# Kernel tuning notes

Hardware: AMD Instinct MI355X
Metric: run time of the kernel (lower is better)

Reference implementation:

```python
import jax, jax.numpy as jnp
import numpy as np

GAMMA = 0.99
BETA = 0.01
B, T, A = 65536, 128, 8


def setup_inputs() -> dict:
    key = jax.random.key(0)
    ks = jax.random.split(key, 6)
    return {
        "values": jax.random.normal(ks[0], (B, T), jnp.float32),
        "last_value": jax.random.normal(ks[1], (B,), jnp.float32),
        "rewards": jax.random.normal(ks[2], (B, T), jnp.float32),
        "log_probs": -jax.nn.softplus(jax.random.normal(ks[3], (B, T, A), jnp.float32)),
        "entropies": jax.random.uniform(ks[4], (B, T, A), jnp.float32),
        "terminal_mask": jax.random.randint(ks[5], (B,), 0, 2) > 0,
    }


def _a3c_loss(values, last_value, rewards, log_probs, entropies, terminal_mask):
    # Bootstrap value R: zero if terminal, else detached last-state value
    R0 = jnp.where(terminal_mask, 0.0, jax.lax.stop_gradient(last_value))  # [B]
    values_next = jnp.concatenate([values[:, 1:], R0[:, None]], axis=1)    # [B,T] = values[i+1]
    lp = log_probs.sum(-1)    # [B,T], log_probs[i].sum()
    ent = entropies.sum(-1)   # [B,T], entropies[i].sum()

    # scan over time (reverse), xs laid out time-major: [T, B]
    xs = (rewards.T, values.T, values_next.T, lp.T, ent.T)
    z = jnp.zeros((values.shape[0],), values.dtype)

    def step(carry, x):
        R, gae, actor, critic = carry
        r, v, v_next, l, e = x
        R = GAMMA * R + r
        adv = R - v
        critic = critic + 0.5 * adv * adv
        delta = r + GAMMA * v_next - v
        gae = gae * GAMMA + delta
        actor = actor - l * jax.lax.stop_gradient(gae) - BETA * e
        return (R, gae, actor, critic), None

    (R, gae, actor, critic), _ = jax.lax.scan(step, (R0, z, z, z), xs, reverse=True)
    return jnp.stack([actor, critic], axis=-1)  # [B, 2]: (actor_loss, critic_loss)


def reference(values, last_value, rewards, log_probs, entropies, terminal_mask):
    return _a3c_loss(values, last_value, rewards, log_probs, entropies, terminal_mask)
```

## Files before the change

kernel.cpp:

```cpp
#include <hip/hip_runtime.h>

#define GAMMA 0.99f
#define BETA  0.01f

typedef const __attribute__((address_space(1))) void GVoid;
typedef __attribute__((address_space(3))) void LVoid;

__global__ __launch_bounds__(256, 4) void a3c_loss_kernel(
    const float* __restrict__ values,
    const float* __restrict__ last_value,
    const float* __restrict__ rewards,
    const float* __restrict__ log_probs,
    const float* __restrict__ entropies,
    const int*   __restrict__ terminal_mask,
    float* __restrict__ out,
    int B)
{
    __shared__ float lds_stage[4][2048];

    const int wave = threadIdx.x >> 6;
    const int lane = threadIdx.x & 63;
    const int b = blockIdx.x * 4 + wave;
    if (b >= B) return;

    const float2 v2 = reinterpret_cast<const float2*>(values  + (size_t)b * 128)[lane];
    const float2 r2 = reinterpret_cast<const float2*>(rewards + (size_t)b * 128)[lane];
    const float lv  = last_value[b];
    const int   tm  = terminal_mask[b];

    const float4* lp4 = reinterpret_cast<const float4*>(log_probs + (size_t)b * 1024);
    const float4* en4 = reinterpret_cast<const float4*>(entropies + (size_t)b * 1024);
    float* wbase = &lds_stage[wave][0];
    #pragma unroll
    for (int k = 0; k < 4; ++k) {
        __builtin_amdgcn_global_load_lds((GVoid*)(lp4 + lane + 64 * k),
                                         (LVoid*)(wbase + 256 * k + lane * 4),
                                         16, 0, 0);
    }
    #pragma unroll
    for (int k = 0; k < 4; ++k) {
        __builtin_amdgcn_global_load_lds((GVoid*)(en4 + lane + 64 * k),
                                         (LVoid*)(wbase + 1024 + 256 * k + lane * 4),
                                         16, 0, 0);
    }
    __builtin_amdgcn_sched_barrier(0);

    const float v0 = v2.x, v1 = v2.y;
    const float r0 = r2.x, r1 = r2.y;

    const float R0 = (tm != 0) ? 0.0f : lv;

    float vnext1 = __shfl_down(v0, 1, 64);
    if (lane == 63) vnext1 = R0;
    const float delta1 = r1 + GAMMA * vnext1 - v1;
    const float delta0 = r0 + GAMMA * v1    - v0;

    float m  = GAMMA * GAMMA;
    float cR = fmaf(GAMMA, r1, r0);
    float cG = fmaf(GAMMA, delta1, delta0);

    #pragma unroll
    for (int d = 1; d < 64; d <<= 1) {
        const float om  = __shfl_down(m,  d, 64);
        const float ocR = __shfl_down(cR, d, 64);
        const float ocG = __shfl_down(cG, d, 64);
        if (lane + d < 64) {
            cR = fmaf(m, ocR, cR);
            cG = fmaf(m, ocG, cG);
            m  = m * om;
        }
    }
    float pm  = __shfl_down(m,  1, 64);
    float pcR = __shfl_down(cR, 1, 64);
    float pcG = __shfl_down(cG, 1, 64);
    if (lane == 63) { pm = 1.0f; pcR = 0.0f; pcG = 0.0f; }

    const float Rin = fmaf(pm, R0, pcR);
    const float gin = pcG;

    const float R1   = fmaf(GAMMA, Rin, r1);
    const float Rt0  = fmaf(GAMMA, R1,  r0);
    const float adv1 = R1  - v1;
    const float adv0 = Rt0 - v0;
    float critic = 0.5f * (adv1 * adv1 + adv0 * adv0);

    const float g1 = fmaf(GAMMA, gin, delta1);
    const float g0 = fmaf(GAMMA, g1,  delta0);

    const int par = (lane >> 1) & 1;
    const int hb  = lane >> 2;
    const int h1 = hb + 16;
    const int h2 = hb + 32;
    const int h3 = hb + 48;
    const float gA0 = __shfl(g0, hb, 64), gB0 = __shfl(g1, hb, 64);
    const float gA1 = __shfl(g0, h1, 64), gB1 = __shfl(g1, h1, 64);
    const float gA2 = __shfl(g0, h2, 64), gB2 = __shfl(g1, h2, 64);
    const float gA3 = __shfl(g0, h3, 64), gB3 = __shfl(g1, h3, 64);
    const float gk0 = par ? gB0 : gA0;
    const float gk1 = par ? gB1 : gA1;
    const float gk2 = par ? gB2 : gA2;
    const float gk3 = par ? gB3 : gA3;

    asm volatile("s_waitcnt vmcnt(0)" ::: "memory");
    __builtin_amdgcn_sched_barrier(0);

    const float4* lpL = reinterpret_cast<const float4*>(wbase);
    const float4* enL = reinterpret_cast<const float4*>(wbase + 1024);
    const float4 L0 = lpL[lane      ];
    const float4 L1 = lpL[lane +  64];
    const float4 L2 = lpL[lane + 128];
    const float4 L3 = lpL[lane + 192];
    const float4 E0 = enL[lane      ];
    const float4 E1 = enL[lane +  64];
    const float4 E2 = enL[lane + 128];
    const float4 E3 = enL[lane + 192];

    const float sL0 = (L0.x + L0.y) + (L0.z + L0.w);
    const float sL1 = (L1.x + L1.y) + (L1.z + L1.w);
    const float sL2 = (L2.x + L2.y) + (L2.z + L2.w);
    const float sL3 = (L3.x + L3.y) + (L3.z + L3.w);
    float actor = -(sL0 * gk0 + sL1 * gk1 + sL2 * gk2 + sL3 * gk3);

    const float esum = ((E0.x + E0.y) + (E0.z + E0.w)) + ((E1.x + E1.y) + (E1.z + E1.w))
                     + ((E2.x + E2.y) + (E2.z + E2.w)) + ((E3.x + E3.y) + (E3.z + E3.w));
    actor = fmaf(-BETA, esum, actor);

    #pragma unroll
    for (int d = 32; d >= 1; d >>= 1) {
        actor  += __shfl_down(actor,  d, 64);
        critic += __shfl_down(critic, d, 64);
    }

    if (lane == 0) {
        reinterpret_cast<float2*>(out)[b] = make_float2(actor, critic);
    }
}

extern "C" void kernel_launch(void* const* d_in, const int* in_sizes, int n_in,
                              void* d_out, int out_size, void* d_ws, size_t ws_size,
                              hipStream_t stream) {
    const float* values      = (const float*)d_in[0];
    const float* last_value  = (const float*)d_in[1];
    const float* rewards     = (const float*)d_in[2];
    const float* log_probs   = (const float*)d_in[3];
    const float* entropies   = (const float*)d_in[4];
    const int*   terminal    = (const int*)d_in[5];
    float* out = (float*)d_out;

    const int B = in_sizes[1];
    const int blocks = (B + 3) / 4;

    a3c_loss_kernel<<<blocks, 256, 0, stream>>>(
        values, last_value, rewards, log_probs, entropies, terminal, out, B);
}
```

Measured before the change: 539.5 us.

## Process 32 rows per wave with double-buffered async LDS staging

Each wave now handles 32 consecutive rows instead of one. It uses two LDS buffers, so the async global-to-LDS loads for the next row (log_probs, entropies, values, rewards, last_value, mask) are in flight while the current row's scan and reduction run. The launch grid shrinks by 32x and occupancy is lowered to 2 blocks per CU to fit the doubled LDS footprint. This amortises launch and scheduling overhead and overlaps memory with compute. The cost is fewer concurrent waves, which can reduce the memory parallelism available to the hardware.

```diff
diff --git a/kernel.cpp b/kernel.cpp
--- a/kernel.cpp
+++ b/kernel.cpp
@@ -6,7 +6,15 @@
 typedef const __attribute__((address_space(1))) void GVoid;
 typedef __attribute__((address_space(3))) void LVoid;
 
-__global__ __launch_bounds__(256, 4) void a3c_loss_kernel(
+#define BUF_FLOATS 2432
+#define ROWS_PER_WAVE 32
+
+#define WAITV(N) do { \
+    asm volatile("s_waitcnt vmcnt(" #N ")" ::: "memory"); \
+    __builtin_amdgcn_sched_barrier(0); \
+} while (0)
+
+__global__ __launch_bounds__(256, 2) void a3c_loss_kernel(
     const float* __restrict__ values,
     const float* __restrict__ last_value,
     const float* __restrict__ rewards,
@@ -16,124 +24,148 @@
     float* __restrict__ out,
     int B)
 {
-    __shared__ float lds_stage[4][2048];
+    __shared__ float lds[4][2][BUF_FLOATS];
 
     const int wave = threadIdx.x >> 6;
     const int lane = threadIdx.x & 63;
-    const int b = blockIdx.x * 4 + wave;
-    if (b >= B) return;
+    const int wid  = blockIdx.x * 4 + wave;
+    const int r0   = wid * ROWS_PER_WAVE;
+    if (r0 >= B) return;
 
-    const float2 v2 = reinterpret_cast<const float2*>(values  + (size_t)b * 128)[lane];
-    const float2 r2 = reinterpret_cast<const float2*>(rewards + (size_t)b * 128)[lane];
-    const float lv  = last_value[b];
-    const int   tm  = terminal_mask[b];
+    float* const buf0 = &lds[wave][0][0];
+    float* const buf1 = &lds[wave][1][0];
 
-    const float4* lp4 = reinterpret_cast<const float4*>(log_probs + (size_t)b * 1024);
-    const float4* en4 = reinterpret_cast<const float4*>(entropies + (size_t)b * 1024);
-    float* wbase = &lds_stage[wave][0];
-    #pragma unroll
-    for (int k = 0; k < 4; ++k) {
-        __builtin_amdgcn_global_load_lds((GVoid*)(lp4 + lane + 64 * k),
-                                         (LVoid*)(wbase + 256 * k + lane * 4),
-                                         16, 0, 0);
+    auto stage = [&](float* buf, int row) {
+        row = (row < B) ? row : (B - 1);
+        const size_t rb = (size_t)row;
+        const float4* lp4 = reinterpret_cast<const float4*>(log_probs + rb * 1024) + lane;
+        const float4* en4 = reinterpret_cast<const float4*>(entropies + rb * 1024) + lane;
+        #pragma unroll
+        for (int k = 0; k < 4; ++k)
+            __builtin_amdgcn_global_load_lds((GVoid*)(lp4 + 64 * k),
+                                             (LVoid*)(buf + 256 * k), 16, 0, 0);
+        #pragma unroll
+        for (int k = 0; k < 4; ++k)
+            __builtin_amdgcn_global_load_lds((GVoid*)(en4 + 64 * k),
+                                             (LVoid*)(buf + 1024 + 256 * k), 16, 0, 0);
+        const float* vp = values  + rb * 128 + lane;
+        const float* rp = rewards + rb * 128 + lane;
+        __builtin_amdgcn_global_load_lds((GVoid*)(vp     ), (LVoid*)(buf + 2048     ), 4, 0, 0);
+        __builtin_amdgcn_global_load_lds((GVoid*)(vp + 64), (LVoid*)(buf + 2048 + 64), 4, 0, 0);
+        __builtin_amdgcn_global_load_lds((GVoid*)(rp     ), (LVoid*)(buf + 2176     ), 4, 0, 0);
+        __builtin_amdgcn_global_load_lds((GVoid*)(rp + 64), (LVoid*)(buf + 2176 + 64), 4, 0, 0);
+        __builtin_amdgcn_global_load_lds((GVoid*)(last_value    + rb), (LVoid*)(buf + 2304), 4, 0, 0);
+        __builtin_amdgcn_global_load_lds((GVoid*)(terminal_mask + rb), (LVoid*)(buf + 2368), 4, 0, 0);
+        __builtin_amdgcn_sched_barrier(0);
+    };
+
+    auto process = [&](const float* buf, int row) {
+        const float2 v2 = reinterpret_cast<const float2*>(buf + 2048)[lane];
+        const float2 r2 = reinterpret_cast<const float2*>(buf + 2176)[lane];
+        const float  lv = buf[2304 + lane];
+        const int    tm = reinterpret_cast<const int*>(buf)[2368 + lane];
+
+        const float v0 = v2.x, v1 = v2.y;
+        const float r0v = r2.x, r1v = r2.y;
+
+        const float R0 = (tm != 0) ? 0.0f : lv;
+
+        float vnext1 = __shfl_down(v0, 1, 64);
+        if (lane == 63) vnext1 = R0;
+        const float delta1 = r1v + GAMMA * vnext1 - v1;
+        const float delta0 = r0v + GAMMA * v1    - v0;
+
+        float m  = GAMMA * GAMMA;
+        float cR = fmaf(GAMMA, r1v, r0v);
+        float cG = fmaf(GAMMA, delta1, delta0);
+
+        #pragma unroll
+        for (int d = 1; d < 64; d <<= 1) {
+            const float om  = __shfl_down(m,  d, 64);
+            const float ocR = __shfl_down(cR, d, 64);
+            const float ocG = __shfl_down(cG, d, 64);
+            if (lane + d < 64) {
+                cR = fmaf(m, ocR, cR);
+                cG = fmaf(m, ocG, cG);
+                m  = m * om;
+            }
+        }
+        float pm  = __shfl_down(m,  1, 64);
+        float pcR = __shfl_down(cR, 1, 64);
+        float pcG = __shfl_down(cG, 1, 64);
+        if (lane == 63) { pm = 1.0f; pcR = 0.0f; pcG = 0.0f; }
+
+        const float Rin = fmaf(pm, R0, pcR);
+        const float gin = pcG;
+
+        const float R1   = fmaf(GAMMA, Rin, r1v);
+        const float Rt0  = fmaf(GAMMA, R1,  r0v);
+        const float adv1 = R1  - v1;
+        const float adv0 = Rt0 - v0;
+        float critic = 0.5f * (adv1 * adv1 + adv0 * adv0);
+
+        const float g1 = fmaf(GAMMA, gin, delta1);
+        const float g0 = fmaf(GAMMA, g1,  delta0);
+
+        const int par = (lane >> 1) & 1;
+        const int hb  = lane >> 2;
+        const float gA0 = __shfl(g0, hb,      64), gB0 = __shfl(g1, hb,      64);
+        const float gA1 = __shfl(g0, hb + 16, 64), gB1 = __shfl(g1, hb + 16, 64);
+        const float gA2 = __shfl(g0, hb + 32, 64), gB2 = __shfl(g1, hb + 32, 64);
+        const float gA3 = __shfl(g0, hb + 48, 64), gB3 = __shfl(g1, hb + 48, 64);
+        const float gk0 = par ? gB0 : gA0;
+        const float gk1 = par ? gB1 : gA1;
+        const float gk2 = par ? gB2 : gA2;
+        const float gk3 = par ? gB3 : gA3;
+
+        const float4* lpL = reinterpret_cast<const float4*>(buf);
+        const float4* enL = reinterpret_cast<const float4*>(buf + 1024);
+        const float4 L0 = lpL[lane      ];
+        const float4 L1 = lpL[lane +  64];
+        const float4 L2 = lpL[lane + 128];
+        const float4 L3 = lpL[lane + 192];
+        const float4 E0 = enL[lane      ];
+        const float4 E1 = enL[lane +  64];
+        const float4 E2 = enL[lane + 128];
+        const float4 E3 = enL[lane + 192];
+
+        const float sL0 = (L0.x + L0.y) + (L0.z + L0.w);
+        const float sL1 = (L1.x + L1.y) + (L1.z + L1.w);
+        const float sL2 = (L2.x + L2.y) + (L2.z + L2.w);
+        const float sL3 = (L3.x + L3.y) + (L3.z + L3.w);
+        float actor = -(sL0 * gk0 + sL1 * gk1 + sL2 * gk2 + sL3 * gk3);
+
+        const float esum = ((E0.x + E0.y) + (E0.z + E0.w)) + ((E1.x + E1.y) + (E1.z + E1.w))
+                         + ((E2.x + E2.y) + (E2.z + E2.w)) + ((E3.x + E3.y) + (E3.z + E3.w));
+        actor = fmaf(-BETA, esum, actor);
+
+        #pragma unroll
+        for (int d = 32; d >= 1; d >>= 1) {
+            actor  += __shfl_down(actor,  d, 64);
+            critic += __shfl_down(critic, d, 64);
+        }
+
+        if (lane == 0 && row < B) {
+            reinterpret_cast<float2*>(out)[row] = make_float2(actor, critic);
+        }
+        __builtin_amdgcn_sched_barrier(0);
+    };
+
+    stage(buf0, r0);
+    #pragma unroll 1
+    for (int i = 0; i < ROWS_PER_WAVE - 2; i += 2) {
+        stage(buf1, r0 + i + 1);
+        WAITV(14);
+        process(buf0, r0 + i);
+        stage(buf0, r0 + i + 2);
+        WAITV(14);
+        process(buf1, r0 + i + 1);
     }
-    #pragma unroll
-    for (int k = 0; k < 4; ++k) {
-        __builtin_amdgcn_global_load_lds((GVoid*)(en4 + lane + 64 * k),
-                                         (LVoid*)(wbase + 1024 + 256 * k + lane * 4),
-                                         16, 0, 0);
-    }
-    __builtin_amdgcn_sched_barrier(0);
-
-    const float v0 = v2.x, v1 = v2.y;
-    const float r0 = r2.x, r1 = r2.y;
-
-    const float R0 = (tm != 0) ? 0.0f : lv;
-
-    float vnext1 = __shfl_down(v0, 1, 64);
-    if (lane == 63) vnext1 = R0;
-    const float delta1 = r1 + GAMMA * vnext1 - v1;
-    const float delta0 = r0 + GAMMA * v1    - v0;
-
-    float m  = GAMMA * GAMMA;
-    float cR = fmaf(GAMMA, r1, r0);
-    float cG = fmaf(GAMMA, delta1, delta0);
-
-    #pragma unroll
-    for (int d = 1; d < 64; d <<= 1) {
-        const float om  = __shfl_down(m,  d, 64);
-        const float ocR = __shfl_down(cR, d, 64);
-        const float ocG = __shfl_down(cG, d, 64);
-        if (lane + d < 64) {
-            cR = fmaf(m, ocR, cR);
-            cG = fmaf(m, ocG, cG);
-            m  = m * om;
-        }
-    }
-    float pm  = __shfl_down(m,  1, 64);
-    float pcR = __shfl_down(cR, 1, 64);
-    float pcG = __shfl_down(cG, 1, 64);
-    if (lane == 63) { pm = 1.0f; pcR = 0.0f; pcG = 0.0f; }
-
-    const float Rin = fmaf(pm, R0, pcR);
-    const float gin = pcG;
-
-    const float R1   = fmaf(GAMMA, Rin, r1);
-    const float Rt0  = fmaf(GAMMA, R1,  r0);
-    const float adv1 = R1  - v1;
-    const float adv0 = Rt0 - v0;
-    float critic = 0.5f * (adv1 * adv1 + adv0 * adv0);
-
-    const float g1 = fmaf(GAMMA, gin, delta1);
-    const float g0 = fmaf(GAMMA, g1,  delta0);
-
-    const int par = (lane >> 1) & 1;
-    const int hb  = lane >> 2;
-    const int h1 = hb + 16;
-    const int h2 = hb + 32;
-    const int h3 = hb + 48;
-    const float gA0 = __shfl(g0, hb, 64), gB0 = __shfl(g1, hb, 64);
-    const float gA1 = __shfl(g0, h1, 64), gB1 = __shfl(g1, h1, 64);
-    const float gA2 = __shfl(g0, h2, 64), gB2 = __shfl(g1, h2, 64);
-    const float gA3 = __shfl(g0, h3, 64), gB3 = __shfl(g1, h3, 64);
-    const float gk0 = par ? gB0 : gA0;
-    const float gk1 = par ? gB1 : gA1;
-    const float gk2 = par ? gB2 : gA2;
-    const float gk3 = par ? gB3 : gA3;
-
-    asm volatile("s_waitcnt vmcnt(0)" ::: "memory");
-    __builtin_amdgcn_sched_barrier(0);
-
-    const float4* lpL = reinterpret_cast<const float4*>(wbase);
-    const float4* enL = reinterpret_cast<const float4*>(wbase + 1024);
-    const float4 L0 = lpL[lane      ];
-    const float4 L1 = lpL[lane +  64];
-    const float4 L2 = lpL[lane + 128];
-    const float4 L3 = lpL[lane + 192];
-    const float4 E0 = enL[lane      ];
-    const float4 E1 = enL[lane +  64];
-    const float4 E2 = enL[lane + 128];
-    const float4 E3 = enL[lane + 192];
-
-    const float sL0 = (L0.x + L0.y) + (L0.z + L0.w);
-    const float sL1 = (L1.x + L1.y) + (L1.z + L1.w);
-    const float sL2 = (L2.x + L2.y) + (L2.z + L2.w);
-    const float sL3 = (L3.x + L3.y) + (L3.z + L3.w);
-    float actor = -(sL0 * gk0 + sL1 * gk1 + sL2 * gk2 + sL3 * gk3);
-
-    const float esum = ((E0.x + E0.y) + (E0.z + E0.w)) + ((E1.x + E1.y) + (E1.z + E1.w))
-                     + ((E2.x + E2.y) + (E2.z + E2.w)) + ((E3.x + E3.y) + (E3.z + E3.w));
-    actor = fmaf(-BETA, esum, actor);
-
-    #pragma unroll
-    for (int d = 32; d >= 1; d >>= 1) {
-        actor  += __shfl_down(actor,  d, 64);
-        critic += __shfl_down(critic, d, 64);
-    }
-
-    if (lane == 0) {
-        reinterpret_cast<float2*>(out)[b] = make_float2(actor, critic);
-    }
+    stage(buf1, r0 + ROWS_PER_WAVE - 1);
+    WAITV(14);
+    process(buf0, r0 + ROWS_PER_WAVE - 2);
+    WAITV(0);
+    process(buf1, r0 + ROWS_PER_WAVE - 1);
 }
 
 extern "C" void kernel_launch(void* const* d_in, const int* in_sizes, int n_in,
@@ -148,8 +180,7 @@
     float* out = (float*)d_out;
 
     const int B = in_sizes[1];
-    const int blocks = (B + 3) / 4;
-
+    const int blocks = (B + 127) / 128;
     a3c_loss_kernel<<<blocks, 256, 0, stream>>>(
         values, last_value, rewards, log_probs, entropies, terminal, out, B);
 }
```

After: 550.9 us. 2.1% more time.
